# Performance work log

Hardware: AMD Instinct MI355X
Metric: run time of the kernel (lower is better)

Reference implementation:

```python
import jax, jax.numpy as jnp
import numpy as np

ENTROPY_THRESHOLD = 4.5
FREQUENCY_THRESHOLD = 0.1


def setup_inputs() -> dict:
    key = jax.random.key(0)
    k1, = jax.random.split(key, 1)
    B, S, D = 4, 4096, 1024
    embeddings = jax.random.normal(k1, (B, S, D), dtype=jnp.float32)
    attention_mask = jnp.ones((B, S), dtype=jnp.int32)
    return {"embeddings": embeddings, "attention_mask": attention_mask}


def _token_entropy(embeddings):
    # F.normalize(dim=-1): x / max(||x||_2, 1e-12)
    norm = jnp.linalg.norm(embeddings, axis=-1, keepdims=True)
    normalized = embeddings / jnp.maximum(norm, 1e-12)
    # [B,S,S] cosine-similarity matrix
    sims = jnp.einsum("bsd,btd->bst", normalized, normalized)
    probs = jax.nn.softmax(sims, axis=-1)
    return -jnp.sum(probs * jnp.log(probs + 1e-10), axis=-1)  # [B,S]


def _frequency_ratio(embeddings):
    mag = jnp.abs(jnp.fft.fft(embeddings, axis=1))  # FFT over seq axis
    max_mag = jnp.max(mag, axis=-1)                 # [B,S]
    mean_mag = jnp.mean(mag, axis=-1)               # [B,S]
    return max_mag / (mean_mag + 1e-10)


def reference(embeddings, attention_mask):
    entropy = _token_entropy(embeddings)            # [B,S]
    freq_ratio = _frequency_ratio(embeddings)       # [B,S]
    entropy_anom = (entropy < ENTROPY_THRESHOLD).astype(jnp.float32)
    freq_anom = (freq_ratio > FREQUENCY_THRESHOLD).astype(jnp.float32)
    scores = (entropy_anom + freq_anom) / 2.0
    return jnp.mean(scores, axis=1, keepdims=True)  # [B,1]
```

## Files before the change

### kernel.cpp

```cpp
#include <hip/hip_runtime.h>
#include <stdint.h>

#define BATCH 4
#define SEQ   4096
#define DIM   1024
#define NTILE (SEQ / 128)
#define NPAIR (NTILE * (NTILE + 1) / 2)
#define KSTEPS (DIM / 128)

typedef int   int4v  __attribute__((ext_vector_type(4)));
typedef int   int8v  __attribute__((ext_vector_type(8)));
typedef float f32x4  __attribute__((ext_vector_type(4)));

__global__ void __launch_bounds__(256) wm_normalize_kernel(const float* __restrict__ emb,
                                                           unsigned char* __restrict__ nrm,
                                                           float* __restrict__ zwreg) {
    const int row = blockIdx.x;
    const int t   = threadIdx.x;
    if (row < 128) zwreg[row * 256 + t] = 0.f;
    const float4 v = reinterpret_cast<const float4*>(emb + (size_t)row * DIM)[t];
    float ss = v.x*v.x + v.y*v.y + v.z*v.z + v.w*v.w;
    #pragma unroll
    for (int off = 32; off >= 1; off >>= 1)
        ss += __shfl_xor(ss, off, 64);
    __shared__ float wsum[4];
    if ((t & 63) == 0) wsum[t >> 6] = ss;
    __syncthreads();
    const float tot   = wsum[0] + wsum[1] + wsum[2] + wsum[3];
    const float scale = 1.0f / fmaxf(sqrtf(tot), 1e-12f);
    int p = __builtin_amdgcn_cvt_pk_fp8_f32(v.x * scale, v.y * scale, 0, false);
    p     = __builtin_amdgcn_cvt_pk_fp8_f32(v.z * scale, v.w * scale, p, true);
    reinterpret_cast<int*>(nrm + (size_t)row * DIM)[t] = p;
}

__global__ void __launch_bounds__(256) wm_entropy_gemm_kernel(const unsigned char* __restrict__ nrm,
                                                              float* __restrict__ Zacc,
                                                              float* __restrict__ Wacc) {
    const int b = blockIdx.z;

    const int bid = blockIdx.x;
    int idx = (bid & 7) * (NPAIR / 8) + (bid >> 3);

    int I = 0;
    while (idx >= (NTILE - I)) { idx -= (NTILE - I); ++I; }
    const int J = I + idx;

    const int crow0 = I * 128;
    const int ccol0 = J * 128;
    const int t    = threadIdx.x;
    const int lane = t & 63;
    const int w    = t >> 6;
    const int wr   = w >> 1;
    const int wc   = w & 1;
    const int fr   = lane & 15;
    const int kg   = lane >> 4;

    __shared__ __align__(16) unsigned char smem[32768];
    unsigned char* const Abuf = smem;
    unsigned char* const Bbuf = smem + 16384;
    float2* const zwbuf = reinterpret_cast<float2*>(smem);

    const unsigned char* baseA = nrm + ((size_t)b * SEQ + crow0) * DIM;
    const unsigned char* baseB = nrm + ((size_t)b * SEQ + ccol0) * DIM;

    const int srow  = w * 8 + (lane >> 3);
    const int skcol = ((lane & 7) ^ (lane >> 3)) * 16;

#define STAGE(kbase)                                                                                   \
    do {                                                                                               \
        _Pragma("unroll")                                                                              \
        for (int i = 0; i < 4; ++i) {                                                                  \
            const int r_ = i * 32 + srow;                                                              \
            __builtin_amdgcn_global_load_lds(                                                          \
                (const __attribute__((address_space(1))) unsigned int*)(baseA + (size_t)r_ * DIM + (kbase) + skcol), \
                (__attribute__((address_space(3))) unsigned int*)(Abuf + i * 4096 + w * 1024),         \
                16, 0, 0);                                                                             \
            __builtin_amdgcn_global_load_lds(                                                          \
                (const __attribute__((address_space(1))) unsigned int*)(baseB + (size_t)r_ * DIM + (kbase) + skcol), \
                (__attribute__((address_space(3))) unsigned int*)(Bbuf + i * 4096 + w * 1024),         \
                16, 0, 0);                                                                             \
        }                                                                                              \
    } while (0)

#define ZV4 {0.f, 0.f, 0.f, 0.f}
    f32x4 c00 = ZV4, c01 = ZV4, c02 = ZV4, c03 = ZV4;
    f32x4 c10 = ZV4, c11 = ZV4, c12 = ZV4, c13 = ZV4;
    f32x4 c20 = ZV4, c21 = ZV4, c22 = ZV4, c23 = ZV4;
    f32x4 c30 = ZV4, c31 = ZV4, c32 = ZV4, c33 = ZV4;

    const int xr  = fr & 7;
    const int g0  = ((kg * 2)     ^ xr) << 4;
    const int g1  = ((kg * 2 + 1) ^ xr) << 4;

#define LD32(buf, rowbyte)                                                                   \
    ({                                                                                       \
        const int4v lo_ = *reinterpret_cast<const int4v*>(&buf[(rowbyte) + g0]);             \
        const int4v hi_ = *reinterpret_cast<const int4v*>(&buf[(rowbyte) + g1]);             \
        (int8v){lo_[0], lo_[1], lo_[2], lo_[3], hi_[0], hi_[1], hi_[2], hi_[3]};             \
    })

#define MX(A, B, C) C = __builtin_amdgcn_mfma_scale_f32_16x16x128_f8f6f4(A, B, C, 0, 0, 0, 0x7F7F7F7F, 0, 0x7F7F7F7F)

    const int rA = (wr * 64 + fr) * 128;
    const int rB = (wc * 64 + fr) * 128;

    for (int tk = 0; tk < KSTEPS; ++tk) {
        STAGE(tk * 128);
        __syncthreads();

        const int8v a0 = LD32(Abuf, rA);
        const int8v a1 = LD32(Abuf, rA + 16 * 128);
        const int8v a2 = LD32(Abuf, rA + 32 * 128);
        const int8v a3 = LD32(Abuf, rA + 48 * 128);
        const int8v b0 = LD32(Bbuf, rB);
        const int8v b1 = LD32(Bbuf, rB + 16 * 128);
        const int8v b2 = LD32(Bbuf, rB + 32 * 128);
        const int8v b3 = LD32(Bbuf, rB + 48 * 128);

        __builtin_amdgcn_s_setprio(1);
        MX(a0, b0, c00);  MX(a0, b1, c01);  MX(a0, b2, c02);  MX(a0, b3, c03);
        MX(a1, b0, c10);  MX(a1, b1, c11);  MX(a1, b2, c12);  MX(a1, b3, c13);
        MX(a2, b0, c20);  MX(a2, b1, c21);  MX(a2, b2, c22);  MX(a2, b3, c23);
        MX(a3, b0, c30);  MX(a3, b1, c31);  MX(a3, b2, c32);  MX(a3, b3, c33);
        __builtin_amdgcn_s_setprio(0);

        __syncthreads();
    }
#undef STAGE
#undef LD32
#undef MX

    float zc0 = 0.f, wv0 = 0.f, zc1 = 0.f, wv1 = 0.f;
    float zc2 = 0.f, wv2 = 0.f, zc3 = 0.f, wv3 = 0.f;

#define REDROW(M, R, A0, A1, A2, A3) do {                                       \
        const float s0_ = (A0)[R], s1_ = (A1)[R], s2_ = (A2)[R], s3_ = (A3)[R]; \
        const float e0_ = __expf(s0_ - 1.0f), e1_ = __expf(s1_ - 1.0f);         \
        const float e2_ = __expf(s2_ - 1.0f), e3_ = __expf(s3_ - 1.0f);         \
        zc0 += e0_;  wv0 += e0_ * s0_;  zc1 += e1_;  wv1 += e1_ * s1_;          \
        zc2 += e2_;  wv2 += e2_ * s2_;  zc3 += e3_;  wv3 += e3_ * s3_;          \
        const int row_ = wr * 64 + (M) * 16 + kg * 4 + (R);                     \
        zwbuf[wc * 2048 + row_ * 16 + fr] =                                     \
            make_float2((e0_ + e1_) + (e2_ + e3_),                              \
                        (e0_ * s0_ + e1_ * s1_) + (e2_ * s2_ + e3_ * s3_));     \
    } while (0)

#define REDROW4(M, A0, A1, A2, A3)                                              \
    REDROW(M, 0, A0, A1, A2, A3); REDROW(M, 1, A0, A1, A2, A3);                 \
    REDROW(M, 2, A0, A1, A2, A3); REDROW(M, 3, A0, A1, A2, A3);

    REDROW4(0, c00, c01, c02, c03)
    REDROW4(1, c10, c11, c12, c13)
    REDROW4(2, c20, c21, c22, c23)
    REDROW4(3, c30, c31, c32, c33)
#undef REDROW4
#undef REDROW

    __syncthreads();

    if (t < 128) {
        float zs = 0.f, ws_ = 0.f;
        #pragma unroll
        for (int j = 0; j < 16; ++j) {
            const int jj = (j + t) & 15;
            const float2 v = zwbuf[t * 16 + jj];
            const float2 u = zwbuf[2048 + t * 16 + jj];
            zs += v.x + u.x;  ws_ += v.y + u.y;
        }
        atomicAdd(&Zacc[b * SEQ + crow0 + t], zs);
        atomicAdd(&Wacc[b * SEQ + crow0 + t], ws_);
    }

    if (I < J) {
        float z0 = zc0, u0 = wv0, z1 = zc1, u1 = wv1;
        float z2 = zc2, u2 = wv2, z3 = zc3, u3 = wv3;
        z0 += __shfl_xor(z0, 16, 64);  u0 += __shfl_xor(u0, 16, 64);
        z0 += __shfl_xor(z0, 32, 64);  u0 += __shfl_xor(u0, 32, 64);
        z1 += __shfl_xor(z1, 16, 64);  u1 += __shfl_xor(u1, 16, 64);
        z1 += __shfl_xor(z1, 32, 64);  u1 += __shfl_xor(u1, 32, 64);
        z2 += __shfl_xor(z2, 16, 64);  u2 += __shfl_xor(u2, 16, 64);
        z2 += __shfl_xor(z2, 32, 64);  u2 += __shfl_xor(u2, 32, 64);
        z3 += __shfl_xor(z3, 16, 64);  u3 += __shfl_xor(u3, 16, 64);
        z3 += __shfl_xor(z3, 32, 64);  u3 += __shfl_xor(u3, 32, 64);
        if (lane < 16) {
            const int c0_ = ccol0 + wc * 64 + lane;
            atomicAdd(&Zacc[b * SEQ + c0_],      z0);
            atomicAdd(&Wacc[b * SEQ + c0_],      u0);
            atomicAdd(&Zacc[b * SEQ + c0_ + 16], z1);
            atomicAdd(&Wacc[b * SEQ + c0_ + 16], u1);
            atomicAdd(&Zacc[b * SEQ + c0_ + 32], z2);
            atomicAdd(&Wacc[b * SEQ + c0_ + 32], u2);
            atomicAdd(&Zacc[b * SEQ + c0_ + 48], z3);
            atomicAdd(&Wacc[b * SEQ + c0_ + 48], u3);
        }
    }
}

__global__ void __launch_bounds__(256) wm_finalize_kernel(const float* __restrict__ Zacc,
                                                          const float* __restrict__ Wacc,
                                                          float* __restrict__ out) {
    const int b = blockIdx.x;
    const int t = threadIdx.x;
    int cnt = 0;
    for (int s = t; s < SEQ; s += 256) {
        const float z  = Zacc[b * SEQ + s];
        const float wv = Wacc[b * SEQ + s];
        const float ent = 1.0f + logf(z) - wv / z;
        cnt += (ent < 4.5f) ? 1 : 0;
    }
    #pragma unroll
    for (int off = 32; off >= 1; off >>= 1)
        cnt += __shfl_xor(cnt, off, 64);
    __shared__ int wcnt[4];
    if ((t & 63) == 0) wcnt[t >> 6] = cnt;
    __syncthreads();
    if (t == 0) {
        const int tot = wcnt[0] + wcnt[1] + wcnt[2] + wcnt[3];
        out[b] = 0.5f + 0.5f * (float)tot / (float)SEQ;
    }
}

extern "C" void kernel_launch(void* const* d_in, const int* in_sizes, int n_in,
                              void* d_out, int out_size, void* d_ws, size_t ws_size,
                              hipStream_t stream) {
    const float* emb = (const float*)d_in[0];

    unsigned char* nrm = (unsigned char*)d_ws;
    const size_t nrm_bytes = (size_t)BATCH * SEQ * DIM;
    float* Zacc = (float*)((char*)d_ws + nrm_bytes);
    float* Wacc = Zacc + BATCH * SEQ;

    wm_normalize_kernel<<<BATCH * SEQ, 256, 0, stream>>>(emb, nrm, Zacc);
    wm_entropy_gemm_kernel<<<dim3(NPAIR, 1, BATCH), 256, 0, stream>>>(nrm, Zacc, Wacc);
    wm_finalize_kernel<<<BATCH, 256, 0, stream>>>(Zacc, Wacc, (float*)d_out);
}
```

Before: 78.59 us.

## Double-buffer LDS tiles to overlap global loads with MFMA compute

Doubles the shared-memory staging area to two A/B buffer pairs and prefetches the next k-step's FP8 tiles via global_load_lds while the current tile is consumed by MFMAs. Explicit vmcnt waits and raw barriers replace __syncthreads to wait only on the older stage. This hides global-load latency at the cost of doubling LDS per block, which can reduce the number of resident blocks per CU.

```diff
diff --git a/kernel.cpp b/kernel.cpp
--- a/kernel.cpp
+++ b/kernel.cpp
@@ -55,9 +55,7 @@
     const int fr   = lane & 15;
     const int kg   = lane >> 4;
 
-    __shared__ __align__(16) unsigned char smem[32768];
-    unsigned char* const Abuf = smem;
-    unsigned char* const Bbuf = smem + 16384;
+    __shared__ __align__(16) unsigned char smem[65536];
     float2* const zwbuf = reinterpret_cast<float2*>(smem);
 
     const unsigned char* baseA = nrm + ((size_t)b * SEQ + crow0) * DIM;
@@ -66,18 +64,18 @@
     const int srow  = w * 8 + (lane >> 3);
     const int skcol = ((lane & 7) ^ (lane >> 3)) * 16;
 
-#define STAGE(kbase)                                                                                   \
+#define STAGE(sel, kbase)                                                                              \
     do {                                                                                               \
         _Pragma("unroll")                                                                              \
         for (int i = 0; i < 4; ++i) {                                                                  \
             const int r_ = i * 32 + srow;                                                              \
             __builtin_amdgcn_global_load_lds(                                                          \
                 (const __attribute__((address_space(1))) unsigned int*)(baseA + (size_t)r_ * DIM + (kbase) + skcol), \
-                (__attribute__((address_space(3))) unsigned int*)(Abuf + i * 4096 + w * 1024),         \
+                (__attribute__((address_space(3))) unsigned int*)(smem + (sel) * 32768 + i * 4096 + w * 1024),       \
                 16, 0, 0);                                                                             \
             __builtin_amdgcn_global_load_lds(                                                          \
                 (const __attribute__((address_space(1))) unsigned int*)(baseB + (size_t)r_ * DIM + (kbase) + skcol), \
-                (__attribute__((address_space(3))) unsigned int*)(Bbuf + i * 4096 + w * 1024),         \
+                (__attribute__((address_space(3))) unsigned int*)(smem + (sel) * 32768 + 16384 + i * 4096 + w * 1024), \
                 16, 0, 0);                                                                             \
         }                                                                                              \
     } while (0)
@@ -92,10 +90,10 @@
     const int g0  = ((kg * 2)     ^ xr) << 4;
     const int g1  = ((kg * 2 + 1) ^ xr) << 4;
 
-#define LD32(buf, rowbyte)                                                                   \
+#define LD32(base, rowbyte)                                                                  \
     ({                                                                                       \
-        const int4v lo_ = *reinterpret_cast<const int4v*>(&buf[(rowbyte) + g0]);             \
-        const int4v hi_ = *reinterpret_cast<const int4v*>(&buf[(rowbyte) + g1]);             \
+        const int4v lo_ = *reinterpret_cast<const int4v*>((base) + (rowbyte) + g0);          \
+        const int4v hi_ = *reinterpret_cast<const int4v*>((base) + (rowbyte) + g1);          \
         (int8v){lo_[0], lo_[1], lo_[2], lo_[3], hi_[0], hi_[1], hi_[2], hi_[3]};             \
     })
 
@@ -104,18 +102,29 @@
     const int rA = (wr * 64 + fr) * 128;
     const int rB = (wc * 64 + fr) * 128;
 
+    STAGE(0, 0);
+    int cur = 0;
     for (int tk = 0; tk < KSTEPS; ++tk) {
-        STAGE(tk * 128);
-        __syncthreads();
-
-        const int8v a0 = LD32(Abuf, rA);
-        const int8v a1 = LD32(Abuf, rA + 16 * 128);
-        const int8v a2 = LD32(Abuf, rA + 32 * 128);
-        const int8v a3 = LD32(Abuf, rA + 48 * 128);
-        const int8v b0 = LD32(Bbuf, rB);
-        const int8v b1 = LD32(Bbuf, rB + 16 * 128);
-        const int8v b2 = LD32(Bbuf, rB + 32 * 128);
-        const int8v b3 = LD32(Bbuf, rB + 48 * 128);
+        if (tk + 1 < KSTEPS) {
+            STAGE(cur ^ 1, (tk + 1) * 128);
+            asm volatile("s_waitcnt vmcnt(8)" ::: "memory");
+        } else {
+            asm volatile("s_waitcnt vmcnt(0)" ::: "memory");
+        }
+        __builtin_amdgcn_sched_barrier(0);
+        __builtin_amdgcn_s_barrier();
+        __builtin_amdgcn_sched_barrier(0);
+
+        const unsigned char* const Ab = smem + cur * 32768;
+        const unsigned char* const Bb = Ab + 16384;
+        const int8v a0 = LD32(Ab, rA);
+        const int8v a1 = LD32(Ab, rA + 16 * 128);
+        const int8v a2 = LD32(Ab, rA + 32 * 128);
+        const int8v a3 = LD32(Ab, rA + 48 * 128);
+        const int8v b0 = LD32(Bb, rB);
+        const int8v b1 = LD32(Bb, rB + 16 * 128);
+        const int8v b2 = LD32(Bb, rB + 32 * 128);
+        const int8v b3 = LD32(Bb, rB + 48 * 128);
 
         __builtin_amdgcn_s_setprio(1);
         MX(a0, b0, c00);  MX(a0, b1, c01);  MX(a0, b2, c02);  MX(a0, b3, c03);
@@ -124,7 +133,10 @@
         MX(a3, b0, c30);  MX(a3, b1, c31);  MX(a3, b2, c32);  MX(a3, b3, c33);
         __builtin_amdgcn_s_setprio(0);
 
-        __syncthreads();
+        __builtin_amdgcn_sched_barrier(0);
+        __builtin_amdgcn_s_barrier();
+        __builtin_amdgcn_sched_barrier(0);
+        cur ^= 1;
     }
 #undef STAGE
 #undef LD32
```

New measurement: 72.99 us. -7.1%, faster.
